# Kernel tuning notes

Measured on AMD Instinct MI355X. Metric: run time of the kernel, lower is better.

## Reference

```python
import jax, jax.numpy as jnp
import numpy as np

N_NODES = 50000
N_EDGES = 500000
D_FEAT = 128


def setup_inputs() -> dict:
    key = jax.random.key(0)
    k1, k2, k3 = jax.random.split(key, 3)
    r = jax.random.normal(k1, (N_NODES, D_FEAT), dtype=jnp.float32)
    e = jax.random.normal(k2, (N_EDGES, D_FEAT), dtype=jnp.float32)
    a = jax.random.randint(k3, (N_EDGES, 2), 0, N_NODES, dtype=jnp.int64)
    return {"r": r, "e": e, "a": a}


def reference(r, e, a):
    # message: gather source/target node features along edges, scale by edge feats
    rij = r[a[:, 0]] * e  # [E, D] messages src -> dst
    rji = r[a[:, 1]] * e  # [E, D] messages dst -> src
    # aggregate: scatter_add into node dimension (fixed num_segments for jit)
    out = jax.ops.segment_sum(rij, a[:, 1], num_segments=r.shape[0])
    out = out + jax.ops.segment_sum(rji, a[:, 0], num_segments=r.shape[0])
    return out  # [N, D]
```

## Files before the change

kernel.cpp:

```cpp
#include <hip/hip_runtime.h>
#include <hip/hip_fp16.h>


#define D_FEAT 128
#define SCAN_TILE 1024
#define CHUNK 8192
#define G_GRP 8

typedef float vf2 __attribute__((ext_vector_type(2)));
typedef float vf4 __attribute__((ext_vector_type(4)));
typedef unsigned long long ull_t;

__device__ inline unsigned pack_h2(float a, float b) {
    __half2 h;
    h.x = __float2half_rn(a);
    h.y = __float2half_rn(b);
    return *reinterpret_cast<unsigned*>(&h);
}
__device__ inline float2 unpack_h2(unsigned u) {
    __half2 h = *reinterpret_cast<__half2*>(&u);
    return __half22float2(h);
}

__global__ __launch_bounds__(256) void hist1_kernel(
    const int* __restrict__ a, unsigned* __restrict__ ghist,
    int n_entries, int nwords) {
    extern __shared__ unsigned h[];
    for (int i = threadIdx.x; i < nwords; i += blockDim.x) h[i] = 0u;
    __syncthreads();
    int s = blockIdx.x * CHUNK;
    int e = s + CHUNK;
    if (e > n_entries) e = n_entries;
    for (int idx = s + threadIdx.x; idx < e; idx += blockDim.x) {
        int n = a[idx];
        atomicAdd(&h[n >> 2], 1u << ((n & 3) * 8));
    }
    __syncthreads();
    unsigned* dst = ghist + (size_t)blockIdx.x * nwords;
    for (int i = threadIdx.x; i < nwords; i += blockDim.x) dst[i] = h[i];
}

__global__ void m2a_kernel(const unsigned* __restrict__ ghist,
                           const float* __restrict__ r,
                           unsigned char* __restrict__ base,
                           unsigned char* __restrict__ gsum,
                           uint2* __restrict__ r16,
                           int n_nodes, int nblk, int gblk, int nwords,
                           int n_r4) {
    int n = blockIdx.x * blockDim.x + threadIdx.x;
    if (n < n_nodes) {
        int g = blockIdx.y;
        int b0 = g * gblk;
        int b1 = b0 + gblk;
        if (b1 > nblk) b1 = nblk;
        int w = n >> 2, sh = (n & 3) * 8;
        int run = 0;
        for (int b = b0; b < b1; ++b) {
            base[(size_t)b * n_nodes + n] = (unsigned char)run;
            run += (int)((ghist[(size_t)b * nwords + w] >> sh) & 0xffu);
        }
        gsum[(size_t)blockIdx.y * n_nodes + n] = (unsigned char)run;
    }
    int tid = (blockIdx.y * gridDim.x + blockIdx.x) * blockDim.x + threadIdx.x;
    int nth = gridDim.x * gridDim.y * blockDim.x;
    for (int i = tid; i < n_r4; i += nth) {
        const float4 v = ((const float4*)r)[i];
        uint2 p;
        p.x = pack_h2(v.x, v.y);
        p.y = pack_h2(v.z, v.w);
        r16[i] = p;
    }
}

__global__ void m2b_kernel(const unsigned char* __restrict__ gsum,
                           unsigned char* __restrict__ gbase,
                           int* __restrict__ deg, int n_nodes) {
    int n = blockIdx.x * blockDim.x + threadIdx.x;
    if (n >= n_nodes) return;
    int run = 0;
    #pragma unroll
    for (int g = 0; g < G_GRP; ++g) {
        gbase[(size_t)g * n_nodes + n] = (unsigned char)run;
        run += (int)gsum[(size_t)g * n_nodes + n];
    }
    deg[n] = run;
}

__global__ void scanA_kernel(const int* __restrict__ deg, int* __restrict__ bsum,
                             int n) {
    __shared__ int wsum[16];
    int t = threadIdx.x, lane = t & 63, w = t >> 6;
    int i = blockIdx.x * SCAN_TILE + t;
    int v = (i < n) ? deg[i] : 0;
    #pragma unroll
    for (int off = 32; off > 0; off >>= 1) v += __shfl_down(v, off, 64);
    if (lane == 0) wsum[w] = v;
    __syncthreads();
    if (t == 0) {
        int s = 0;
        #pragma unroll
        for (int k = 0; k < 16; ++k) s += wsum[k];
        bsum[blockIdx.x] = s;
    }
}

__global__ void scanB_kernel(int* __restrict__ bsum, int* __restrict__ bbase,
                             int* __restrict__ offs, int nblk, int n) {
    if (threadIdx.x == 0) {
        int run = 0;
        for (int b = 0; b < nblk; ++b) {
            bbase[b] = run;
            run += bsum[b];
        }
        offs[n] = run;
    }
}

__global__ void scanC_kernel(const int* __restrict__ deg, int* __restrict__ offs,
                             const int* __restrict__ bbase, int n) {
    __shared__ int wsum[16];
    int t = threadIdx.x, lane = t & 63, w = t >> 6;
    int i = blockIdx.x * SCAN_TILE + t;
    int v = (i < n) ? deg[i] : 0;
    int x = v;
    #pragma unroll
    for (int off = 1; off < 64; off <<= 1) {
        int y = __shfl_up(x, off, 64);
        if (lane >= off) x += y;
    }
    if (lane == 63) wsum[w] = x;
    __syncthreads();
    if (w == 0 && lane < 16) {
        int s = wsum[lane];
        #pragma unroll
        for (int off = 1; off < 16; off <<= 1) {
            int y = __shfl_up(s, off, 64);
            if (lane >= off) s += y;
        }
        wsum[lane] = s;
    }
    __syncthreads();
    int wbase = (w == 0) ? 0 : wsum[w - 1];
    if (i < n) offs[i] = x - v + wbase + bbase[blockIdx.x];
}

__global__ __launch_bounds__(256) void fill3_kernel(
    const int* __restrict__ a, const int* __restrict__ offs,
    const unsigned char* __restrict__ base,
    const unsigned char* __restrict__ gbase, int2* __restrict__ pl,
    int n_entries, int n_nodes, int nwords, int gblk) {
    extern __shared__ unsigned cur[];
    for (int i = threadIdx.x; i < nwords; i += blockDim.x) cur[i] = 0u;
    __syncthreads();
    int s = blockIdx.x * CHUNK;
    int e = s + CHUNK;
    if (e > n_entries) e = n_entries;
    const unsigned char* brow = base + (size_t)blockIdx.x * n_nodes;
    const unsigned char* grow = gbase + (size_t)(blockIdx.x / gblk) * n_nodes;
    for (int idx = s + threadIdx.x; idx < e; idx += blockDim.x) {
        int other  = a[idx];
        int center = a[idx ^ 1];
        int sh = (center & 3) * 8;
        unsigned old = atomicAdd(&cur[center >> 2], 1u << sh);
        int local = (int)((old >> sh) & 0xffu);
        int pos = offs[center] + (int)grow[center] + (int)brow[center] + local;
        pl[pos] = make_int2(idx >> 1, other);
    }
}

__global__ __launch_bounds__(256) void gather_w2_kernel(
    const unsigned* __restrict__ r16, const float* __restrict__ e,
    const int* __restrict__ offs, const int2* __restrict__ pl,
    float* __restrict__ out, int n_nodes) {
    int n = blockIdx.x * 4 + (threadIdx.x >> 6);
    if (n >= n_nodes) return;
    int lane = threadIdx.x & 63;
    int half = lane >> 5;
    int l32  = lane & 31;
    int start = offs[n];
    int end = offs[n + 1];
    float ax = 0.f, ay = 0.f, az = 0.f, aw = 0.f;
    int i = start;
    #define PAIR_STEP(OFS)                                                    \
        {                                                                     \
            ull_t w = __builtin_nontemporal_load(                             \
                (const ull_t*)(pl + i + (OFS) + half));                       \
            int ei = (int)(unsigned)w;                                        \
            int oi = (int)(w >> 32);                                          \
            vf4 ev = __builtin_nontemporal_load(                              \
                ((const vf4*)(e + (size_t)ei * D_FEAT)) + l32);               \
            uint2 ru = *(((const uint2*)(r16 + (size_t)oi * 64)) + l32);      \
            float2 rlo = unpack_h2(ru.x);                                     \
            float2 rhi = unpack_h2(ru.y);                                     \
            ax += ev.x * rlo.x; ay += ev.y * rlo.y;                           \
            az += ev.z * rhi.x; aw += ev.w * rhi.y;                           \
        }
    for (; i + 8 <= end; i += 8) {
        PAIR_STEP(0)
        PAIR_STEP(2)
        PAIR_STEP(4)
        PAIR_STEP(6)
    }
    for (; i + 2 <= end; i += 2) {
        PAIR_STEP(0)
    }
    if (i < end && half == 0) {
        ull_t w = __builtin_nontemporal_load((const ull_t*)(pl + i));
        int ei = (int)(unsigned)w;
        int oi = (int)(w >> 32);
        vf4 ev = __builtin_nontemporal_load(
            ((const vf4*)(e + (size_t)ei * D_FEAT)) + l32);
        uint2 ru = *(((const uint2*)(r16 + (size_t)oi * 64)) + l32);
        float2 rlo = unpack_h2(ru.x);
        float2 rhi = unpack_h2(ru.y);
        ax += ev.x * rlo.x; ay += ev.y * rlo.y;
        az += ev.z * rhi.x; aw += ev.w * rhi.y;
    }
    #undef PAIR_STEP
    ax += __shfl_xor(ax, 32);
    ay += __shfl_xor(ay, 32);
    az += __shfl_xor(az, 32);
    aw += __shfl_xor(aw, 32);
    if (half == 0) {
        vf4 res;
        res.x = ax; res.y = ay; res.z = az; res.w = aw;
        __builtin_nontemporal_store(
            res, ((vf4*)(out + (size_t)n * D_FEAT)) + l32);
    }
}


__global__ void hist_kernel(const int* __restrict__ a, int* __restrict__ deg,
                            int n_elems) {
    int i = blockIdx.x * blockDim.x + threadIdx.x;
    if (i < n_elems) atomicAdd(&deg[a[i]], 1);
}

__global__ void fill_kernel(const int* __restrict__ a, int* __restrict__ cursor,
                            int2* __restrict__ pl, int n_entries) {
    int k = blockIdx.x * blockDim.x + threadIdx.x;
    if (k >= n_entries) return;
    int edge = k >> 1, j = k & 1;
    int other  = a[2 * edge + j];
    int center = a[2 * edge + (j ^ 1)];
    int pos = atomicAdd(&cursor[center], 1);
    pl[pos] = make_int2(edge, other);
}

__global__ void scanC_cursor_kernel(int* __restrict__ deg, int* __restrict__ offs,
                                    const int* __restrict__ bbase, int n) {
    __shared__ int wsum[16];
    int t = threadIdx.x, lane = t & 63, w = t >> 6;
    int i = blockIdx.x * SCAN_TILE + t;
    int v = (i < n) ? deg[i] : 0;
    int x = v;
    #pragma unroll
    for (int off = 1; off < 64; off <<= 1) {
        int y = __shfl_up(x, off, 64);
        if (lane >= off) x += y;
    }
    if (lane == 63) wsum[w] = x;
    __syncthreads();
    if (w == 0 && lane < 16) {
        int s = wsum[lane];
        #pragma unroll
        for (int off = 1; off < 16; off <<= 1) {
            int y = __shfl_up(s, off, 64);
            if (lane >= off) s += y;
        }
        wsum[lane] = s;
    }
    __syncthreads();
    int wbase = (w == 0) ? 0 : wsum[w - 1];
    if (i < n) {
        int excl = x - v + wbase + bbase[blockIdx.x];
        offs[i] = excl;
        deg[i] = excl;
    }
}

__global__ __launch_bounds__(256) void gather_f32_kernel(
    const float* __restrict__ r, const float* __restrict__ e,
    const int* __restrict__ offs, const int2* __restrict__ pl,
    float* __restrict__ out, int n_nodes) {
    int n = blockIdx.x * 4 + (threadIdx.x >> 6);
    if (n >= n_nodes) return;
    int lane = threadIdx.x & 63;
    int start = offs[n];
    int end = offs[n + 1];
    float accx = 0.f, accy = 0.f;
    for (int i = start; i < end; ++i) {
        int2 p0 = pl[i];
        float2 ev0 = *((const float2*)(e + (size_t)p0.x * D_FEAT) + lane);
        float2 rv0 = *((const float2*)(r + (size_t)p0.y * D_FEAT) + lane);
        accx += ev0.x * rv0.x;
        accy += ev0.y * rv0.y;
    }
    float2 res;
    res.x = accx;
    res.y = accy;
    *((float2*)(out + (size_t)n * D_FEAT) + lane) = res;
}

__global__ void mp_scatter_kernel(const float* __restrict__ r,
                                  const float* __restrict__ e,
                                  const int* __restrict__ a,
                                  float* __restrict__ out,
                                  int n_edges) {
    long long gid = (long long)blockIdx.x * blockDim.x + threadIdx.x;
    int edge = (int)(gid >> 7);
    int feat = (int)(gid & 127);
    if (edge >= n_edges) return;
    int s = a[2 * edge];
    int d = a[2 * edge + 1];
    float ev = e[(long long)edge * D_FEAT + feat];
    float rs = r[(long long)s * D_FEAT + feat];
    float rd = r[(long long)d * D_FEAT + feat];
    atomicAdd(&out[(long long)d * D_FEAT + feat], rs * ev);
    atomicAdd(&out[(long long)s * D_FEAT + feat], rd * ev);
}

extern "C" void kernel_launch(void* const* d_in, const int* in_sizes, int n_in,
                              void* d_out, int out_size, void* d_ws, size_t ws_size,
                              hipStream_t stream) {
    const float* r = (const float*)d_in[0];
    const float* e = (const float*)d_in[1];
    const int*   a = (const int*)d_in[2];
    float* out = (float*)d_out;
    (void)n_in;

    int n_nodes   = in_sizes[0] / D_FEAT;
    int n_edges   = in_sizes[1] / D_FEAT;
    int n_entries = 2 * n_edges;
    int n_r4      = in_sizes[0] / 4;

    int block = 256;
    int grid_e = (n_entries + block - 1) / block;
    int nblk_scan = (n_nodes + SCAN_TILE - 1) / SCAN_TILE;
    int nblk_c = (n_entries + CHUNK - 1) / CHUNK;
    int gblk   = (nblk_c + G_GRP - 1) / G_GRP;
    int nwords = (n_nodes + 3) / 4;
    size_t lds_bytes = (size_t)nwords * sizeof(unsigned);

    {
        size_t ghist_words = (size_t)nblk_c * nwords;
        size_t base_bytes  = (((size_t)nblk_c * n_nodes) + 3) & ~(size_t)3;
        size_t gsum_bytes  = (((size_t)G_GRP * n_nodes) + 3) & ~(size_t)3;
        size_t ints_tail   = (size_t)n_nodes + (size_t)(n_nodes + 1)
                           + 2 * (size_t)nblk_scan;
        size_t head_bytes  = ghist_words * 4 + base_bytes + 2 * gsum_bytes
                           + (size_t)n_r4 * sizeof(uint2) + ints_tail * 4;
        head_bytes = (head_bytes + 7) & ~(size_t)7;
        size_t need = head_bytes + (size_t)n_entries * sizeof(int2);
        if (ws_size >= need && nblk_scan <= 1024 && lds_bytes <= 64 * 1024) {
            unsigned*      ghist = (unsigned*)d_ws;
            unsigned char* basep = (unsigned char*)(ghist + ghist_words);
            unsigned char* gsum  = basep + base_bytes;
            unsigned char* gbase = gsum + gsum_bytes;
            uint2*         r16   = (uint2*)(gbase + gsum_bytes);
            int*           deg   = (int*)(r16 + n_r4);
            int*           offs  = deg + n_nodes;
            int*           bsum  = offs + n_nodes + 1;
            int*           bbase = bsum + nblk_scan;
            int2*          pl    = (int2*)((char*)d_ws + head_bytes);

            hist1_kernel<<<nblk_c, block, lds_bytes, stream>>>(a, ghist,
                                                               n_entries,
                                                               nwords);
            dim3 gm2a((n_nodes + block - 1) / block, G_GRP);
            m2a_kernel<<<gm2a, block, 0, stream>>>(ghist, r, basep, gsum, r16,
                                                   n_nodes, nblk_c, gblk,
                                                   nwords, n_r4);
            int grid_m = (n_nodes + block - 1) / block;
            m2b_kernel<<<grid_m, block, 0, stream>>>(gsum, gbase, deg, n_nodes);
            scanA_kernel<<<nblk_scan, SCAN_TILE, 0, stream>>>(deg, bsum,
                                                              n_nodes);
            scanB_kernel<<<1, 64, 0, stream>>>(bsum, bbase, offs, nblk_scan,
                                               n_nodes);
            scanC_kernel<<<nblk_scan, SCAN_TILE, 0, stream>>>(deg, offs, bbase,
                                                              n_nodes);
            fill3_kernel<<<nblk_c, block, lds_bytes, stream>>>(
                a, offs, basep, gbase, pl, n_entries, n_nodes, nwords, gblk);
            int grid_g = (n_nodes + 3) / 4;
            gather_w2_kernel<<<grid_g, 256, 0, stream>>>(
                (const unsigned*)r16, e, offs, pl, out, n_nodes);
            return;
        }
    }

    {
        size_t ints_head = (size_t)n_nodes + (size_t)(n_nodes + 1)
                         + 2 * (size_t)nblk_scan;
        ints_head = (ints_head + 1) & ~(size_t)1;
        size_t need = ints_head * sizeof(int) + (size_t)n_entries * sizeof(int2);
        if (ws_size >= need && nblk_scan <= 1024) {
            int*  deg  = (int*)d_ws;
            int*  offs = deg + n_nodes;
            int*  bsum = offs + n_nodes + 1;
            int*  bbase= bsum + nblk_scan;
            int2* pl   = (int2*)((int*)d_ws + ints_head);

            hipMemsetAsync(deg, 0, (size_t)n_nodes * sizeof(int), stream);
            hist_kernel<<<grid_e, block, 0, stream>>>(a, deg, n_entries);
            scanA_kernel<<<nblk_scan, SCAN_TILE, 0, stream>>>(deg, bsum, n_nodes);
            scanB_kernel<<<1, 64, 0, stream>>>(bsum, bbase, offs, nblk_scan,
                                               n_nodes);
            scanC_cursor_kernel<<<nblk_scan, SCAN_TILE, 0, stream>>>(deg, offs,
                                                                     bbase,
                                                                     n_nodes);
            fill_kernel<<<grid_e, block, 0, stream>>>(a, deg, pl, n_entries);
            int grid_g = (n_nodes + 3) / 4;
            gather_f32_kernel<<<grid_g, 256, 0, stream>>>(r, e, offs, pl, out,
                                                          n_nodes);
            return;
        }
    }

    hipMemsetAsync(d_out, 0, (size_t)out_size * sizeof(float), stream);
    long long total = (long long)n_edges * D_FEAT;
    long long grid = (total + block - 1) / block;
    mp_scatter_kernel<<<(int)grid, block, 0, stream>>>(r, e, a, out, n_edges);
}
```

Before: 496.3 us.

## Replace three-kernel prefix scan with per-wave atomic segment allocation

Folds the degree computation and the three scan kernels into one kernel. Each wave does an inclusive shuffle scan of node degrees and reserves a contiguous range with a single atomicAdd on a global cursor. Each node then stores a (start,end) pair that fill and gather read. This removes three kernel launches and their serialization, including the single-thread scanB. In exchange, segments are no longer in node order, which can reduce locality in the pl array, and a memset launch is added.

```diff
diff --git a/kernel.cpp b/kernel.cpp
--- a/kernel.cpp
+++ b/kernel.cpp
@@ -7,7 +7,6 @@
 #define CHUNK 8192
 #define G_GRP 8
 
-typedef float vf2 __attribute__((ext_vector_type(2)));
 typedef float vf4 __attribute__((ext_vector_type(4)));
 typedef unsigned long long ull_t;
 
@@ -72,80 +71,37 @@
     }
 }
 
-__global__ void m2b_kernel(const unsigned char* __restrict__ gsum,
+__global__ void m2c_kernel(const unsigned char* __restrict__ gsum,
                            unsigned char* __restrict__ gbase,
-                           int* __restrict__ deg, int n_nodes) {
+                           int2* __restrict__ seg, int* __restrict__ cursor,
+                           int n_nodes) {
     int n = blockIdx.x * blockDim.x + threadIdx.x;
-    if (n >= n_nodes) return;
+    int lane = threadIdx.x & 63;
     int run = 0;
-    #pragma unroll
-    for (int g = 0; g < G_GRP; ++g) {
-        gbase[(size_t)g * n_nodes + n] = (unsigned char)run;
-        run += (int)gsum[(size_t)g * n_nodes + n];
-    }
-    deg[n] = run;
-}
-
-__global__ void scanA_kernel(const int* __restrict__ deg, int* __restrict__ bsum,
-                             int n) {
-    __shared__ int wsum[16];
-    int t = threadIdx.x, lane = t & 63, w = t >> 6;
-    int i = blockIdx.x * SCAN_TILE + t;
-    int v = (i < n) ? deg[i] : 0;
-    #pragma unroll
-    for (int off = 32; off > 0; off >>= 1) v += __shfl_down(v, off, 64);
-    if (lane == 0) wsum[w] = v;
-    __syncthreads();
-    if (t == 0) {
-        int s = 0;
+    if (n < n_nodes) {
         #pragma unroll
-        for (int k = 0; k < 16; ++k) s += wsum[k];
-        bsum[blockIdx.x] = s;
-    }
-}
-
-__global__ void scanB_kernel(int* __restrict__ bsum, int* __restrict__ bbase,
-                             int* __restrict__ offs, int nblk, int n) {
-    if (threadIdx.x == 0) {
-        int run = 0;
-        for (int b = 0; b < nblk; ++b) {
-            bbase[b] = run;
-            run += bsum[b];
-        }
-        offs[n] = run;
-    }
-}
-
-__global__ void scanC_kernel(const int* __restrict__ deg, int* __restrict__ offs,
-                             const int* __restrict__ bbase, int n) {
-    __shared__ int wsum[16];
-    int t = threadIdx.x, lane = t & 63, w = t >> 6;
-    int i = blockIdx.x * SCAN_TILE + t;
-    int v = (i < n) ? deg[i] : 0;
-    int x = v;
+        for (int g = 0; g < G_GRP; ++g) {
+            gbase[(size_t)g * n_nodes + n] = (unsigned char)run;
+            run += (int)gsum[(size_t)g * n_nodes + n];
+        }
+    }
+    int x = run;
     #pragma unroll
     for (int off = 1; off < 64; off <<= 1) {
         int y = __shfl_up(x, off, 64);
         if (lane >= off) x += y;
     }
-    if (lane == 63) wsum[w] = x;
-    __syncthreads();
-    if (w == 0 && lane < 16) {
-        int s = wsum[lane];
-        #pragma unroll
-        for (int off = 1; off < 16; off <<= 1) {
-            int y = __shfl_up(s, off, 64);
-            if (lane >= off) s += y;
-        }
-        wsum[lane] = s;
-    }
-    __syncthreads();
-    int wbase = (w == 0) ? 0 : wsum[w - 1];
-    if (i < n) offs[i] = x - v + wbase + bbase[blockIdx.x];
+    int wbase = 0;
+    if (lane == 63) wbase = atomicAdd(cursor, x);
+    wbase = __shfl(wbase, 63, 64);
+    if (n < n_nodes) {
+        int start = wbase + (x - run);
+        seg[n] = make_int2(start, start + run);
+    }
 }
 
 __global__ __launch_bounds__(256) void fill3_kernel(
-    const int* __restrict__ a, const int* __restrict__ offs,
+    const int* __restrict__ a, const int2* __restrict__ seg,
     const unsigned char* __restrict__ base,
     const unsigned char* __restrict__ gbase, int2* __restrict__ pl,
     int n_entries, int n_nodes, int nwords, int gblk) {
@@ -163,22 +119,23 @@
         int sh = (center & 3) * 8;
         unsigned old = atomicAdd(&cur[center >> 2], 1u << sh);
         int local = (int)((old >> sh) & 0xffu);
-        int pos = offs[center] + (int)grow[center] + (int)brow[center] + local;
+        int pos = seg[center].x + (int)grow[center] + (int)brow[center] + local;
         pl[pos] = make_int2(idx >> 1, other);
     }
 }
 
 __global__ __launch_bounds__(256) void gather_w2_kernel(
     const unsigned* __restrict__ r16, const float* __restrict__ e,
-    const int* __restrict__ offs, const int2* __restrict__ pl,
+    const int2* __restrict__ seg, const int2* __restrict__ pl,
     float* __restrict__ out, int n_nodes) {
     int n = blockIdx.x * 4 + (threadIdx.x >> 6);
     if (n >= n_nodes) return;
     int lane = threadIdx.x & 63;
     int half = lane >> 5;
     int l32  = lane & 31;
-    int start = offs[n];
-    int end = offs[n + 1];
+    int2 sg = seg[n];
+    int start = sg.x;
+    int end = sg.y;
     float ax = 0.f, ay = 0.f, az = 0.f, aw = 0.f;
     int i = start;
     #define PAIR_STEP(OFS)                                                    \
@@ -245,6 +202,36 @@
     int center = a[2 * edge + (j ^ 1)];
     int pos = atomicAdd(&cursor[center], 1);
     pl[pos] = make_int2(edge, other);
+}
+
+__global__ void scanA_kernel(const int* __restrict__ deg, int* __restrict__ bsum,
+                             int n) {
+    __shared__ int wsum[16];
+    int t = threadIdx.x, lane = t & 63, w = t >> 6;
+    int i = blockIdx.x * SCAN_TILE + t;
+    int v = (i < n) ? deg[i] : 0;
+    #pragma unroll
+    for (int off = 32; off > 0; off >>= 1) v += __shfl_down(v, off, 64);
+    if (lane == 0) wsum[w] = v;
+    __syncthreads();
+    if (t == 0) {
+        int s = 0;
+        #pragma unroll
+        for (int k = 0; k < 16; ++k) s += wsum[k];
+        bsum[blockIdx.x] = s;
+    }
+}
+
+__global__ void scanB_kernel(int* __restrict__ bsum, int* __restrict__ bbase,
+                             int* __restrict__ offs, int nblk, int n) {
+    if (threadIdx.x == 0) {
+        int run = 0;
+        for (int b = 0; b < nblk; ++b) {
+            bbase[b] = run;
+            run += bsum[b];
+        }
+        offs[n] = run;
+    }
 }
 
 __global__ void scanC_cursor_kernel(int* __restrict__ deg, int* __restrict__ offs,
@@ -344,26 +331,25 @@
 
     {
         size_t ghist_words = (size_t)nblk_c * nwords;
-        size_t base_bytes  = (((size_t)nblk_c * n_nodes) + 3) & ~(size_t)3;
-        size_t gsum_bytes  = (((size_t)G_GRP * n_nodes) + 3) & ~(size_t)3;
-        size_t ints_tail   = (size_t)n_nodes + (size_t)(n_nodes + 1)
-                           + 2 * (size_t)nblk_scan;
+        size_t base_bytes  = (((size_t)nblk_c * n_nodes) + 7) & ~(size_t)7;
+        size_t gsum_bytes  = (((size_t)G_GRP * n_nodes) + 7) & ~(size_t)7;
         size_t head_bytes  = ghist_words * 4 + base_bytes + 2 * gsum_bytes
-                           + (size_t)n_r4 * sizeof(uint2) + ints_tail * 4;
+                           + (size_t)n_r4 * sizeof(uint2)
+                           + (size_t)n_nodes * sizeof(int2)
+                           + 8;
         head_bytes = (head_bytes + 7) & ~(size_t)7;
         size_t need = head_bytes + (size_t)n_entries * sizeof(int2);
-        if (ws_size >= need && nblk_scan <= 1024 && lds_bytes <= 64 * 1024) {
+        if (ws_size >= need && lds_bytes <= 64 * 1024) {
             unsigned*      ghist = (unsigned*)d_ws;
             unsigned char* basep = (unsigned char*)(ghist + ghist_words);
             unsigned char* gsum  = basep + base_bytes;
             unsigned char* gbase = gsum + gsum_bytes;
             uint2*         r16   = (uint2*)(gbase + gsum_bytes);
-            int*           deg   = (int*)(r16 + n_r4);
-            int*           offs  = deg + n_nodes;
-            int*           bsum  = offs + n_nodes + 1;
-            int*           bbase = bsum + nblk_scan;
+            int2*          seg   = (int2*)(r16 + n_r4);
+            int*           cursor= (int*)(seg + n_nodes);
             int2*          pl    = (int2*)((char*)d_ws + head_bytes);
 
+            hipMemsetAsync(cursor, 0, sizeof(int), stream);
             hist1_kernel<<<nblk_c, block, lds_bytes, stream>>>(a, ghist,
                                                                n_entries,
                                                                nwords);
@@ -372,18 +358,13 @@
                                                    n_nodes, nblk_c, gblk,
                                                    nwords, n_r4);
             int grid_m = (n_nodes + block - 1) / block;
-            m2b_kernel<<<grid_m, block, 0, stream>>>(gsum, gbase, deg, n_nodes);
-            scanA_kernel<<<nblk_scan, SCAN_TILE, 0, stream>>>(deg, bsum,
-                                                              n_nodes);
-            scanB_kernel<<<1, 64, 0, stream>>>(bsum, bbase, offs, nblk_scan,
-                                               n_nodes);
-            scanC_kernel<<<nblk_scan, SCAN_TILE, 0, stream>>>(deg, offs, bbase,
-                                                              n_nodes);
+            m2c_kernel<<<grid_m, block, 0, stream>>>(gsum, gbase, seg, cursor,
+                                                     n_nodes);
             fill3_kernel<<<nblk_c, block, lds_bytes, stream>>>(
-                a, offs, basep, gbase, pl, n_entries, n_nodes, nwords, gblk);
+                a, seg, basep, gbase, pl, n_entries, n_nodes, nwords, gblk);
             int grid_g = (n_nodes + 3) / 4;
             gather_w2_kernel<<<grid_g, 256, 0, stream>>>(
-                (const unsigned*)r16, e, offs, pl, out, n_nodes);
+                (const unsigned*)r16, e, seg, pl, out, n_nodes);
             return;
         }
     }
```

Result: no change. 501.5 us (+1.1%).
